# Kernel optimization log

Measured on AMD Instinct MI355X. Metric: run time of the kernel, lower is better.

Reference implementation:

```python
import jax, jax.numpy as jnp
import numpy as np

T, B, V = 200, 4096, 100000
PAD = 1  # token id 1 is excluded from the bag (vocab pad token)


def setup_inputs() -> dict:
    key = jax.random.key(0)
    k1, k2, k3 = jax.random.split(key, 3)
    text = jax.random.randint(k1, (T, B), 0, V, dtype=jnp.int64)
    W = jax.random.normal(k2, (1, V), dtype=jnp.float32) * 0.02
    b = jax.random.normal(k3, (1,), dtype=jnp.float32) * 0.02
    return {"text": text, "W": W, "b": b}


def _bow(text):
    # text: [T, B] int token ids -> multi-hot bag-of-words [B, V] (set membership)
    tokens = text.T  # [B, T]
    vals = (tokens != PAD).astype(jnp.float32)  # pad writes 0, real tokens write 1
    batch_idx = jnp.arange(tokens.shape[0])[:, None]  # [B, 1]
    bow = jnp.zeros((tokens.shape[0], V), dtype=jnp.float32)
    # scatter-max implements set semantics under duplicate token ids
    return bow.at[batch_idx, tokens].max(vals)


def reference(text, W, b):
    bow = _bow(text)                       # [B, V]
    score = bow @ W.T + b                  # [B, 1]
    return jax.nn.sigmoid(score)
```

## Files before the change

### kernel.cpp

```cpp
#include <hip/hip_runtime.h>
#include <math.h>

#define T_LEN 200
#define B_SZ  4096
#define V_SZ  100000
#define PAD_TOK 1
#define HASH_SIZE 1024

__global__ __launch_bounds__(256) void bow_sigmoid_kernel(
    const int*   __restrict__ text,
    const float* __restrict__ W,
    const float* __restrict__ bias,
    float*       __restrict__ out)
{
    __shared__ int   hset[HASH_SIZE];
    __shared__ float wave_sums[4];

    const int tid = threadIdx.x;

    const int blk = blockIdx.x;
    const int b = (blk & 7) * (B_SZ / 8) + (blk >> 3);

    for (int i = tid; i < HASH_SIZE; i += 256) hset[i] = -1;
    __syncthreads();

    float sum = 0.0f;
    if (tid < T_LEN) {
        const int tok = text[tid * B_SZ + b];
        if (tok != PAD_TOK) {
            unsigned h = ((unsigned)tok * 2654435761u) & (HASH_SIZE - 1);
            for (;;) {
                const int old = atomicCAS(&hset[h], -1, tok);
                if (old == -1) {
                    sum = W[tok];
                    break;
                }
                if (old == tok) break;
                h = (h + 1) & (HASH_SIZE - 1);
            }
        }
    }
    __syncthreads();

    #pragma unroll
    for (int off = 32; off > 0; off >>= 1)
        sum += __shfl_down(sum, off, 64);
    if ((tid & 63) == 0) wave_sums[tid >> 6] = sum;
    __syncthreads();

    if (tid == 0) {
        const float s = wave_sums[0] + wave_sums[1] + wave_sums[2] + wave_sums[3] + bias[0];
        out[b] = 1.0f / (1.0f + expf(-s));
    }
}

extern "C" void kernel_launch(void* const* d_in, const int* in_sizes, int n_in,
                              void* d_out, int out_size, void* d_ws, size_t ws_size,
                              hipStream_t stream) {
    const int*   text = (const int*)d_in[0];
    const float* W    = (const float*)d_in[1];
    const float* bias = (const float*)d_in[2];
    float*       out  = (float*)d_out;

    bow_sigmoid_kernel<<<B_SZ, 256, 0, stream>>>(text, W, bias, out);
}
```

Measured before the change: 64.44 us.

## Process sixteen batch columns per block with per-column shared hash sets

```diff
diff --git a/kernel.cpp b/kernel.cpp
--- a/kernel.cpp
+++ b/kernel.cpp
@@ -1,56 +1,73 @@
 #include <hip/hip_runtime.h>
 #include <math.h>
 
-#define T_LEN 200
-#define B_SZ  4096
-#define V_SZ  100000
+#define T_LEN   200
+#define B_SZ    4096
+#define V_SZ    100000
 #define PAD_TOK 1
-#define HASH_SIZE 1024
 
-__global__ __launch_bounds__(256) void bow_sigmoid_kernel(
+#define G        16
+#define NBLOCKS  (B_SZ / G)
+#define NTHREADS 512
+#define HBITS    9
+#define HSIZE    (1 << HBITS)
+#define ROWS_PER_ITER (NTHREADS / G)
+#define MAX_K    ((T_LEN + ROWS_PER_ITER - 1) / ROWS_PER_ITER)
+
+__global__ __launch_bounds__(NTHREADS) void bow_sigmoid_kernel(
     const int*   __restrict__ text,
     const float* __restrict__ W,
     const float* __restrict__ bias,
     float*       __restrict__ out)
 {
-    __shared__ int   hset[HASH_SIZE];
-    __shared__ float wave_sums[4];
+    __shared__ int   hset[G][HSIZE];
+    __shared__ float acc[G];
 
     const int tid = threadIdx.x;
+    const int blk = blockIdx.x;
 
-    const int blk = blockIdx.x;
-    const int b = (blk & 7) * (B_SZ / 8) + (blk >> 3);
+    const int g  = (blk & 7) * (NBLOCKS / 8) + (blk >> 3);
+    const int b0 = g * G;
 
-    for (int i = tid; i < HASH_SIZE; i += 256) hset[i] = -1;
+    for (int i = tid; i < G * HSIZE; i += NTHREADS) ((int*)hset)[i] = -1;
+    if (tid < G) acc[tid] = 0.0f;
     __syncthreads();
 
+    const int c  = tid & (G - 1);
+    const int t0 = tid >> 4;
+
+    int toks[MAX_K];
+    #pragma unroll
+    for (int k = 0; k < MAX_K; ++k) {
+        const int t = t0 + k * ROWS_PER_ITER;
+        toks[k] = (t < T_LEN) ? text[t * B_SZ + b0 + c] : PAD_TOK;
+    }
+
     float sum = 0.0f;
-    if (tid < T_LEN) {
-        const int tok = text[tid * B_SZ + b];
-        if (tok != PAD_TOK) {
-            unsigned h = ((unsigned)tok * 2654435761u) & (HASH_SIZE - 1);
-            for (;;) {
-                const int old = atomicCAS(&hset[h], -1, tok);
-                if (old == -1) {
-                    sum = W[tok];
-                    break;
-                }
-                if (old == tok) break;
-                h = (h + 1) & (HASH_SIZE - 1);
+    #pragma unroll
+    for (int k = 0; k < MAX_K; ++k) {
+        const int tok = toks[k];
+        if (tok == PAD_TOK) continue;
+        unsigned h = ((unsigned)tok * 2654435761u) >> (32 - HBITS);
+        for (;;) {
+            const int old = atomicCAS(&hset[c][h], -1, tok);
+            if (old == -1) {
+                sum += W[tok];
+                break;
             }
+            if (old == tok) break;
+            h = (h + 1) & (HSIZE - 1);
         }
     }
+
+    sum += __shfl_xor(sum, 16, 64);
+    sum += __shfl_xor(sum, 32, 64);
+    if ((tid & 63) < G) atomicAdd(&acc[c], sum);
     __syncthreads();
 
-    #pragma unroll
-    for (int off = 32; off > 0; off >>= 1)
-        sum += __shfl_down(sum, off, 64);
-    if ((tid & 63) == 0) wave_sums[tid >> 6] = sum;
-    __syncthreads();
-
-    if (tid == 0) {
-        const float s = wave_sums[0] + wave_sums[1] + wave_sums[2] + wave_sums[3] + bias[0];
-        out[b] = 1.0f / (1.0f + expf(-s));
+    if (tid < G) {
+        const float s = acc[tid] + bias[0];
+        out[b0 + tid] = 1.0f / (1.0f + expf(-s));
     }
 }
 
@@ -62,5 +79,5 @@
     const float* bias = (const float*)d_in[2];
     float*       out  = (float*)d_out;
 
-    bow_sigmoid_kernel<<<B_SZ, 256, 0, stream>>>(text, W, bias, out);
+    bow_sigmoid_kernel<<<NBLOCKS, NTHREADS, 0, stream>>>(text, W, bias, out);
 }
```

New measurement: 67.14 us. +4.2%, slower.
